# Kernel tuning notes

Hardware: AMD Instinct MI355X
Metric: run time of the kernel (lower is better)

The kernel has to match this reference:

```python
import jax, jax.numpy as jnp
import numpy as np

SEQ_LEN = 8
NUM_HEADS = 8
LN_EPS = 1e-5
GN_EPS = 64e-5  # GroupNorm eps = head_dim * 1e-5 (RWKV7 convention, head_dim=64)


def layer_norm(x, w, b):
    mu = x.mean(-1, keepdims=True)
    var = ((x - mu) ** 2).mean(-1, keepdims=True)
    return (x - mu) / jnp.sqrt(var + LN_EPS) * w + b


def token_shift(x):
    # delta = shift(x) - x; shift prepends one zero token along time
    return jnp.pad(x, ((0, 0), (1, 0), (0, 0)))[:, :-1] - x


def group_norm(x, w, b, H):
    B, T, C = x.shape
    xh = x.reshape(B, T, H, C // H)
    mu = xh.mean(-1, keepdims=True)
    var = ((xh - mu) ** 2).mean(-1, keepdims=True)
    return ((xh - mu) / jnp.sqrt(var + GN_EPS)).reshape(B, T, C) * w + b


def rwkv7_scan(r, w, k, v, a, b, H):
    # Generalized delta-rule recurrence (RWKV7):
    #   S_t = S_{t-1} * diag(exp(-exp(w_t))) + (S_{t-1} a_t) b_t^T + v_t k_t^T
    #   o_t = S_t r_t
    B, T, C = r.shape
    N = C // H

    def tm(x):  # [B,T,C] -> [T,B,H,N] (time-major for scan)
        return x.reshape(B, T, H, N).transpose(1, 0, 2, 3)

    decay = jnp.exp(-jnp.exp(tm(w)))
    rs, ks, vs, as_, bs = tm(r), tm(k), tm(v), tm(a), tm(b)

    def step(S, inp):
        rt, dt, kt, vt, at, bt = inp  # each [B,H,N]
        sa = jnp.einsum('bhij,bhj->bhi', S, at)
        S = (S * dt[:, :, None, :]
             + sa[..., None] * bt[:, :, None, :]
             + vt[..., None] * kt[:, :, None, :])
        return S, jnp.einsum('bhij,bhj->bhi', S, rt)

    S0 = jnp.zeros((B, H, N, N), r.dtype)
    _, out = jax.lax.scan(step, S0, (rs, decay, ks, vs, as_, bs))
    return out.transpose(1, 0, 2, 3).reshape(B, T, C)


def _forward(image_tensor, pos_emb, xm, w0, w1, w2, a0, a1, a2, v0, v1, v2,
             g1, g2, kkp, kap, rkp, Wr, Wk, Wv, Wo, lnx_w, lnx_b,
             ln1_w, ln1_b, ln2_w, ln2_b, fxk, Wkey, Wval, lnf_w, lnf_b):
    EB, C, ih, iw = image_tensor.shape
    B = EB // SEQ_LEN
    H = NUM_HEADS
    x = image_tensor.transpose(0, 2, 3, 1).reshape(EB, ih * iw, C)
    x = (x + pos_emb).reshape(B, SEQ_LEN * ih * iw, C)  # [B, T, C]
    L = Wr.shape[0]
    v_first = None
    for l in range(L):
        # ---- time mix (RWKV7 attention) ----
        h = layer_norm(x, ln1_w[l], ln1_b[l])
        Bh, T, _ = h.shape
        dx = token_shift(h)
        xr, xw, xk, xv, xa, xg = [h + dx * xm[l, i] for i in range(6)]
        r = xr @ Wr[l]
        w = -jax.nn.softplus(-(w0[l] + jnp.tanh(xw @ w1[l]) @ w2[l])) - 0.5
        k = xk @ Wk[l]
        v = xv @ Wv[l]
        if v_first is None:
            v_first = v
        else:
            v = v + (v_first - v) * jax.nn.sigmoid(v0[l] + (xv @ v1[l]) @ v2[l])
        a = jax.nn.sigmoid(a0[l] + (xa @ a1[l]) @ a2[l])  # in-context lr
        g = jax.nn.sigmoid(xg @ g1[l]) @ g2[l]
        kk = (k * kkp[l]).reshape(Bh, T, H, -1)
        kk = kk / jnp.maximum(jnp.linalg.norm(kk, axis=-1, keepdims=True), 1e-12)
        kk = kk.reshape(Bh, T, C)
        k = k * (1.0 + (a - 1.0) * kap[l])
        o = rwkv7_scan(r, w, k, v, -kk, kk * a, H)
        o = group_norm(o, lnx_w[l], lnx_b[l], H)
        r4, k4, v4 = (t.reshape(Bh, T, H, -1) for t in (r, k, v))
        o = o + ((r4 * k4 * rkp[l]).sum(-1, keepdims=True) * v4).reshape(Bh, T, C)
        x = x + (o * g) @ Wo[l]
        # ---- channel mix (squared-ReLU FFN) ----
        h = layer_norm(x, ln2_w[l], ln2_b[l])
        kf = h + token_shift(h) * fxk[l]
        x = x + jnp.square(jax.nn.relu(kf @ Wkey[l])) @ Wval[l]
    x = layer_norm(x, lnf_w, lnf_b)
    return x.reshape(EB, ih, iw, C).transpose(0, 3, 1, 2)


def setup_inputs() -> dict:
    key = jax.random.key(0)
    ks = jax.random.split(key, 24)
    L, C, H = 8, 512, 8
    DW, DA, DV, DG, FF = 64, 64, 32, 128, 2048
    EB, IV, IW = 32, 8, 16
    FS = IV * IW

    def n(k, shape, s=0.02):
        return jax.random.normal(k, shape, jnp.float32) * s

    return dict(
        image_tensor=jax.random.normal(ks[0], (EB, C, IV, IW), jnp.float32),
        pos_emb=n(ks[1], (1, FS, C)),
        xm=jax.random.uniform(ks[2], (L, 6, C), jnp.float32),
        w0=n(ks[3], (L, C), 0.5) - 0.5,
        w1=n(ks[4], (L, C, DW), 0.02), w2=n(ks[5], (L, DW, C), 0.1),
        a0=jnp.zeros((L, C), jnp.float32),
        a1=n(ks[6], (L, C, DA)), a2=n(ks[7], (L, DA, C), 0.1),
        v0=jnp.ones((L, C), jnp.float32),
        v1=n(ks[8], (L, C, DV)), v2=n(ks[9], (L, DV, C), 0.1),
        g1=n(ks[10], (L, C, DG)), g2=n(ks[11], (L, DG, C), 0.1),
        kkp=jnp.full((L, C), 0.85, jnp.float32),
        kap=jnp.ones((L, C), jnp.float32),
        rkp=n(ks[12], (L, H, C // H), 0.3),
        Wr=n(ks[13], (L, C, C)), Wk=n(ks[14], (L, C, C)),
        Wv=n(ks[15], (L, C, C)), Wo=n(ks[16], (L, C, C)),
        lnx_w=jnp.ones((L, C), jnp.float32), lnx_b=jnp.zeros((L, C), jnp.float32),
        ln1_w=jnp.ones((L, C), jnp.float32), ln1_b=jnp.zeros((L, C), jnp.float32),
        ln2_w=jnp.ones((L, C), jnp.float32), ln2_b=jnp.zeros((L, C), jnp.float32),
        fxk=jax.random.uniform(ks[17], (L, C), jnp.float32),
        Wkey=n(ks[18], (L, C, FF)), Wval=n(ks[19], (L, FF, C)),
        lnf_w=jnp.ones((C,), jnp.float32), lnf_b=jnp.zeros((C,), jnp.float32),
    )


def reference(image_tensor, pos_emb, xm, w0, w1, w2, a0, a1, a2, v0, v1, v2,
              g1, g2, kkp, kap, rkp, Wr, Wk, Wv, Wo, lnx_w, lnx_b,
              ln1_w, ln1_b, ln2_w, ln2_b, fxk, Wkey, Wval, lnf_w, lnf_b):
    return _forward(image_tensor, pos_emb, xm, w0, w1, w2, a0, a1, a2, v0, v1,
                    v2, g1, g2, kkp, kap, rkp, Wr, Wk, Wv, Wo, lnx_w, lnx_b,
                    ln1_w, ln1_b, ln2_w, ln2_b, fxk, Wkey, Wval, lnf_w, lnf_b)
```

## Files before the change

### kernel.cpp

```cpp
#include <hip/hip_runtime.h>
#include <hip/hip_bf16.h>
#include <math.h>


#define NTOK 4096
#define CDIM 512
#define TT   1024
#define LC   64
#define NCH  16
#define TB   8

#define BM 128
#define BK 32

enum { EPI_NONE=0, EPI_TANH, EPI_SIG, EPI_DECAY, EPI_SIGB, EPI_VMIX, EPI_RELU2, EPI_ADD };

typedef short bf16x8 __attribute__((ext_vector_type(8)));
typedef float f32x4 __attribute__((ext_vector_type(4)));
typedef unsigned short ushort_t;

__device__ __forceinline__ float wsum64(float v) {
#pragma unroll
  for (int s = 1; s < 64; s <<= 1) v += __shfl_xor(v, s);
  return v;
// ... 100 lines not shown
  if (nk > 1) STAGE(1, BK);
  int bc = 0, bs = 2;
  for (int k = 0; k + 1 < nk; ++k) {
    asm volatile("s_waitcnt vmcnt(%0)" :: "i"(LPW) : "memory");
    __builtin_amdgcn_s_barrier();
    if (k + 2 < nk) {
      STAGE(bs, (k + 2) * BK);
      bs = (bs == 2) ? 0 : bs + 1;
    }
    COMPUTE(bc);
    bc = (bc == 2) ? 0 : bc + 1;
  }
  asm volatile("s_waitcnt vmcnt(0)" ::: "memory");
  __builtin_amdgcn_s_barrier();
  COMPUTE(bc);
#undef STAGE
#undef COMPUTE

  void* Cout = sg.C;
  const float* bias = sg.bias;
  const float* e1 = sg.e1;
  const int em = m0 + wm + ((lane >> 4) << 2);
  const int en = n0 + wn + (lane & 15);

#define EPI_STORE(EPI_, OBF_)                                                 \
  { _Pragma("unroll") for (int fi = 0; fi < 4; ++fi) {                        \
      _Pragma("unroll") for (int fj = 0; fj < WNF; ++fj) {                    \
        const int gn = en + fj * 16;                                          \
        if (gn < N) {                                                         \
          _Pragma("unroll") for (int rr = 0; rr < 4; ++rr) {                  \
            const int gm = em + fi * 16 + rr;                                 \
            const size_t idx = (size_t)gm * N + gn;                           \
            const float y = acc[fi][fj][rr];                                  \
            float outv;                                                       \
            if (EPI_ == EPI_NONE) { outv = y; }                               \
            else if (EPI_ == EPI_TANH) { outv = tanhf(y); }                   \
            else if (EPI_ == EPI_SIG) { outv = sigm(y); }                     \
            else if (EPI_ == EPI_DECAY) {                                     \
              const float z = bias[gn] + y;                                   \
              const float w = -log1pf(expf(-z)) - 0.5f;                       \
              outv = expf(-expf(w));                                          \
            } else if (EPI_ == EPI_SIGB) { outv = sigm(bias[gn] + y); }       \
            else if (EPI_ == EPI_VMIX) {                                      \
              const float vr = ((float*)Cout)[idx];                           \
              outv = vr + (e1[idx] - vr) * sigm(bias[gn] + y);                \
            } else if (EPI_ == EPI_RELU2) {                                   \
              const float t = fmaxf(y, 0.f); outv = t * t;                    \
            } else { outv = ((float*)Cout)[idx] + y; }                        \
            if (OBF_) ((ushort_t*)Cout)[idx] = f2bf(outv);                    \
            else      ((float*)Cout)[idx] = outv;                             \
          }                                                                   \
        }                                                                     \
      } } }

  switch (sg.epi) {
    case EPI_NONE:  if (sg.obf) EPI_STORE(EPI_NONE, 1) else EPI_STORE(EPI_NONE, 0); break;
    case EPI_TANH:  EPI_STORE(EPI_TANH, 1); break;
    case EPI_SIG:   EPI_STORE(EPI_SIG, 1); break;
    case EPI_DECAY: EPI_STORE(EPI_DECAY, 0); break;
    case EPI_SIGB:  EPI_STORE(EPI_SIGB, 0); break;
    case EPI_VMIX:  EPI_STORE(EPI_VMIX, 0); break;
    case EPI_RELU2: EPI_STORE(EPI_RELU2, 1); break;
    case EPI_ADD:   EPI_STORE(EPI_ADD, 0); break;
  }
#undef EPI_STORE
}

__global__ __launch_bounds__(256) void wprep_k(
    const float* __restrict__ in, ushort_t* __restrict__ out,
    int K, int N, int Npad)
{
  __shared__ float t[32][33];
  const int l = blockIdx.z;
  const int n0 = blockIdx.x * 32, k0 = blockIdx.y * 32;
  const int tx = threadIdx.x & 31, ty = threadIdx.x >> 5;
  const float* src = in + (size_t)l * K * N;
  ushort_t* dst = out + (size_t)l * Npad * K;
#pragma unroll
  for (int i = 0; i < 32; i += 8) {
    const int k = k0 + ty + i, n = n0 + tx;
    t[ty + i][tx] = (n < N) ? src[(size_t)k * N + n] : 0.f;
  }
  __syncthreads();
#pragma unroll
  for (int i = 0; i < 32; i += 8) {
    const int n = n0 + ty + i, k = k0 + tx;
    dst[(size_t)n * K + k] = f2bf(t[tx][ty + i]);
  }
}

__global__ __launch_bounds__(256) void lnmix6_k(
    const float* __restrict__ x, const float* __restrict__ w,
    const float* __restrict__ b, const float* __restrict__ xml,
    ushort_t* __restrict__ xr, ushort_t* __restrict__ xw,
    ushort_t* __restrict__ xk, ushort_t* __restrict__ xv,
    ushort_t* __restrict__ xa, ushort_t* __restrict__ xg)
{
  const int m = blockIdx.x * 4 + (threadIdx.x >> 6);
  const int lane = threadIdx.x & 63;
  const int c0 = lane << 3;
  const size_t idx = (size_t)m * CDIM + c0;
  const bool first = ((m & (TT - 1)) == 0);
  float v[8], p[8];
  *(float4*)&v[0] = *(const float4*)&x[idx];
  *(float4*)&v[4] = *(const float4*)&x[idx + 4];
  if (first) {
#pragma unroll
    for (int j = 0; j < 8; ++j) p[j] = 0.f;
  } else {
    *(float4*)&p[0] = *(const float4*)&x[idx - CDIM];
    *(float4*)&p[4] = *(const float4*)&x[idx - CDIM + 4];
  }
  float s = 0.f, sp = 0.f;
#pragma unroll
  for (int j = 0; j < 8; ++j) { s += v[j]; sp += p[j]; }
  s = wsum64(s); sp = wsum64(sp);
  const float mu = s * (1.f / 512.f), mup = sp * (1.f / 512.f);
  float q = 0.f, qp = 0.f;
#pragma unroll
  for (int j = 0; j < 8; ++j) {
    const float d1 = v[j] - mu, d2 = p[j] - mup;
    q += d1 * d1; qp += d2 * d2;
  }
  q = wsum64(q); qp = wsum64(qp);
  const float is = rsqrtf(q * (1.f / 512.f) + 1e-5f);
  const float isp = rsqrtf(qp * (1.f / 512.f) + 1e-5f);
  float wc[8], bc[8];
  *(float4*)&wc[0] = *(const float4*)&w[c0]; *(float4*)&wc[4] = *(const float4*)&w[c0 + 4];
  *(float4*)&bc[0] = *(const float4*)&b[c0]; *(float4*)&bc[4] = *(const float4*)&b[c0 + 4];
  float hv[8], dx[8];
#pragma unroll
  for (int j = 0; j < 8; ++j) {
    hv[j] = (v[j] - mu) * is * wc[j] + bc[j];
    const float hp = first ? 0.f : (p[j] - mup) * isp * wc[j] + bc[j];
    dx[j] = hp - hv[j];
  }
  ushort_t* outs[6] = {xr, xw, xk, xv, xa, xg};
#pragma unroll
  for (int o = 0; o < 6; ++o) {
    float mc[8];
    *(float4*)&mc[0] = *(const float4*)&xml[o * CDIM + c0];
    *(float4*)&mc[4] = *(const float4*)&xml[o * CDIM + c0 + 4];
    bf16x8 pk;
#pragma unroll
    for (int j = 0; j < 8; ++j) pk[j] = (short)f2bf(fmaf(dx[j], mc[j], hv[j]));
    *(bf16x8*)&outs[o][idx] = pk;
  }
}

__global__ __launch_bounds__(256) void lnmix1_k(
    const float* __restrict__ x, const float* __restrict__ w,
    const float* __restrict__ b, const float* __restrict__ coef,
    ushort_t* __restrict__ kf)
{
  const int m = blockIdx.x * 4 + (threadIdx.x >> 6);
  const int lane = threadIdx.x & 63;
  const int c0 = lane << 3;
  const size_t idx = (size_t)m * CDIM + c0;
  const bool first = ((m & (TT - 1)) == 0);
  float v[8], p[8];
  *(float4*)&v[0] = *(const float4*)&x[idx];
  *(float4*)&v[4] = *(const float4*)&x[idx + 4];
  if (first) {
#pragma unroll
    for (int j = 0; j < 8; ++j) p[j] = 0.f;
  } else {
    *(float4*)&p[0] = *(const float4*)&x[idx - CDIM];
    *(float4*)&p[4] = *(const float4*)&x[idx - CDIM + 4];
  }
  float s = 0.f, sp = 0.f;
#pragma unroll
  for (int j = 0; j < 8; ++j) { s += v[j]; sp += p[j]; }
  s = wsum64(s); sp = wsum64(sp);
  const float mu = s * (1.f / 512.f), mup = sp * (1.f / 512.f);
  float q = 0.f, qp = 0.f;
#pragma unroll
  for (int j = 0; j < 8; ++j) {
    const float d1 = v[j] - mu, d2 = p[j] - mup;
    q += d1 * d1; qp += d2 * d2;
  }
  q = wsum64(q); qp = wsum64(qp);
  const float is = rsqrtf(q * (1.f / 512.f) + 1e-5f);
  const float isp = rsqrtf(qp * (1.f / 512.f) + 1e-5f);
  bf16x8 pk;
#pragma unroll
  for (int j = 0; j < 8; ++j) {
    const float wc = w[c0 + j], bc = b[c0 + j];
    const float hv = (v[j] - mu) * is * wc + bc;
    const float hp = first ? 0.f : (p[j] - mup) * isp * wc + bc;
    pk[j] = (short)f2bf(fmaf(hp - hv, coef[c0 + j], hv));
  }
  *(bf16x8*)&kf[idx] = pk;
}

__global__ __launch_bounds__(256) void prep_k(
    float* __restrict__ k, const float* __restrict__ a,
    const float* __restrict__ kkp, const float* __restrict__ kap,
    float* __restrict__ aa, float* __restrict__ bb)
{
  const int m = blockIdx.x * 4 + (threadIdx.x >> 6);
  const int lane = threadIdx.x & 63;
  const int c0 = lane << 3;
  const size_t idx = (size_t)m * CDIM + c0;
  float kv[8], av[8], kp[8], ka[8];
  *(float4*)&kv[0] = *(const float4*)&k[idx];     *(float4*)&kv[4] = *(const float4*)&k[idx + 4];
  *(float4*)&av[0] = *(const float4*)&a[idx];     *(float4*)&av[4] = *(const float4*)&a[idx + 4];
  *(float4*)&kp[0] = *(const float4*)&kkp[c0];    *(float4*)&kp[4] = *(const float4*)&kkp[c0 + 4];
  *(float4*)&ka[0] = *(const float4*)&kap[c0];    *(float4*)&ka[4] = *(const float4*)&kap[c0 + 4];
  float kk[8], ss = 0.f;
#pragma unroll
  for (int j = 0; j < 8; ++j) { kk[j] = kv[j] * kp[j]; ss += kk[j] * kk[j]; }
  ss = gsum8(ss);
  const float rden = 1.f / fmaxf(sqrtf(ss), 1e-12f);
  float oaa[8], obb[8], okk[8];
#pragma unroll
  for (int j = 0; j < 8; ++j) {
    const float kkn = kk[j] * rden;
    oaa[j] = -kkn;
    obb[j] = kkn * av[j];
    okk[j] = kv[j] * (1.f + (av[j] - 1.f) * ka[j]);
  }
  *(float4*)&aa[idx] = *(float4*)&oaa[0]; *(float4*)&aa[idx + 4] = *(float4*)&oaa[4];
  *(float4*)&bb[idx] = *(float4*)&obb[0]; *(float4*)&bb[idx + 4] = *(float4*)&obb[4];
  *(float4*)&k[idx]  = *(float4*)&okk[0]; *(float4*)&k[idx + 4]  = *(float4*)&okk[4];
}

__global__ __launch_bounds__(256) void post_k(
    const float* __restrict__ o, const float* __restrict__ r,
    const float* __restrict__ k, const float* __restrict__ v,
    const float* __restrict__ g, const float* __restrict__ gw,
    const float* __restrict__ gb, const float* __restrict__ rkp,
    ushort_t* __restrict__ og)
{
  const int m = blockIdx.x * 4 + (threadIdx.x >> 6);
  const int lane = threadIdx.x & 63;
  const int c0 = lane << 3;
  const size_t idx = (size_t)m * CDIM + c0;
  float ov[8], rv[8], kv[8], vv[8], gv[8], rp[8];
  *(float4*)&ov[0] = *(const float4*)&o[idx];   *(float4*)&ov[4] = *(const float4*)&o[idx + 4];
  *(float4*)&rv[0] = *(const float4*)&r[idx];   *(float4*)&rv[4] = *(const float4*)&r[idx + 4];
  *(float4*)&kv[0] = *(const float4*)&k[idx];   *(float4*)&kv[4] = *(const float4*)&k[idx + 4];
  *(float4*)&vv[0] = *(const float4*)&v[idx];   *(float4*)&vv[4] = *(const float4*)&v[idx + 4];
  *(float4*)&gv[0] = *(const float4*)&g[idx];   *(float4*)&gv[4] = *(const float4*)&g[idx + 4];
  *(float4*)&rp[0] = *(const float4*)&rkp[c0];  *(float4*)&rp[4] = *(const float4*)&rkp[c0 + 4];
  float s = 0.f, dot = 0.f;
#pragma unroll
  for (int j = 0; j < 8; ++j) { s += ov[j]; dot += rv[j] * kv[j] * rp[j]; }
  s = gsum8(s); dot = gsum8(dot);
  const float mu = s * (1.f / 64.f);
  float q = 0.f;
#pragma unroll
  for (int j = 0; j < 8; ++j) { const float d = ov[j] - mu; q += d * d; }
  q = gsum8(q);
  const float is = rsqrtf(q * (1.f / 64.f) + 64e-5f);
  bf16x8 pk;
#pragma unroll
  for (int j = 0; j < 8; ++j) {
    const float gn = (ov[j] - mu) * is * gw[c0 + j] + gb[c0 + j];
    pk[j] = (short)f2bf((gn + dot * vv[j]) * gv[j]);
  }
  *(bf16x8*)&og[idx] = pk;
}

__global__ __launch_bounds__(512) void ln_final_k(
    const float* __restrict__ x, const float* __restrict__ w,
    const float* __restrict__ b, float* __restrict__ out)
{
  const int m = blockIdx.x, c = threadIdx.x;
  const size_t idx = (size_t)m * CDIM + c;
  const float v = x[idx];
  __shared__ float red[8], red2[8];
  float s = wsum64(v);
  if ((c & 63) == 0) red[c >> 6] = s;
  __syncthreads();
  float tot = 0.f;
#pragma unroll
  for (int u = 0; u < 8; ++u) tot += red[u];
  const float mu = tot * (1.f / 512.f);
  const float dv = v - mu;
  float s2 = wsum64(dv * dv);
  if ((c & 63) == 0) red2[c >> 6] = s2;
  __syncthreads();
  float vt = 0.f;
#pragma unroll
  for (int u = 0; u < 8; ++u) vt += red2[u];
  const float y = dv * rsqrtf(vt * (1.f / 512.f) + 1e-5f) * w[c] + b[c];
  const int bidx = m >> 10, t = m & 1023;
  const int p = t & 127, eb = bidx * 8 + (t >> 7);
  out[((size_t)eb * CDIM + c) * 128 + p] = y;
}

__global__ __launch_bounds__(512) void build_x_k(
    const float* __restrict__ img, const float* __restrict__ pos,
    float* __restrict__ x)
{
  const int m = blockIdx.x, c = threadIdx.x;
  const int bidx = m >> 10, t = m & 1023;
  const int p = t & 127, eb = bidx * 8 + (t >> 7);
  x[(size_t)m * CDIM + c] =
      img[((size_t)eb * CDIM + c) * 128 + p] + pos[(size_t)p * CDIM + c];
}

__global__ __launch_bounds__(256) void scan1_k(
    const float* __restrict__ d, const float* __restrict__ k,
    const float* __restrict__ v, const float* __restrict__ aa,
    const float* __restrict__ bb,
    float* __restrict__ P, float* __restrict__ Q)
{
  const int ch = blockIdx.x, bh = blockIdx.y;
  const int b = bh >> 3, hh = bh & 7;
  const int tid = threadIdx.x;
  const int rg = tid >> 4, cg = tid & 15;
  const int r0 = rg << 2, c0 = cg << 2;
  float S[16], Pr[16];
#pragma unroll
  for (int ri = 0; ri < 4; ++ri)
#pragma unroll
    for (int cj = 0; cj < 4; ++cj) {
      S[ri * 4 + cj] = 0.f;
      Pr[ri * 4 + cj] = (r0 + ri == c0 + cj) ? 1.f : 0.f;
    }

  __shared__ float sbuf[3][5 * TB * 64];
  const size_t base = (size_t)b * TT * CDIM + (size_t)ch * LC * CDIM + hh * 64;
  const float* srcs[5] = {d, k, v, aa, bb};
  const int f0 = tid, f1 = tid + 256, f2 = tid + 512;
  const float* gp0 = srcs[f0 >> 7] + base + (size_t)((f0 >> 4) & 7) * CDIM + ((f0 & 15) << 2);
  const float* gp1 = srcs[f1 >> 7] + base + (size_t)((f1 >> 4) & 7) * CDIM + ((f1 & 15) << 2);
  const float* gp2 = (tid < 128)
      ? srcs[f2 >> 7] + base + (size_t)((f2 >> 4) & 7) * CDIM + ((f2 & 15) << 2)
      : srcs[0];

#define STAGE1(bf_, goff_)                                     \
  {                                                            \
    glds16(gp0 + (goff_), &sbuf[bf_][f0 << 2]);                \
    glds16(gp1 + (goff_), &sbuf[bf_][f1 << 2]);                \
    if (tid < 128) glds16(gp2 + (goff_), &sbuf[bf_][f2 << 2]); \
  }

#define CGRP1(bf_)                                                              \
  {                                                                             \
    const float* sb0 = sbuf[bf_];                                               \
    _Pragma("unroll") for (int tt = 0; tt < TB; ++tt) {                         \
      const float* sd  = sb0 + 0 * TB * 64 + tt * 64;                           \
      const float* sk  = sb0 + 1 * TB * 64 + tt * 64;                           \
      const float* sv  = sb0 + 2 * TB * 64 + tt * 64;                           \
      const float* sa  = sb0 + 3 * TB * 64 + tt * 64;                           \
      const float* sbv = sb0 + 4 * TB * 64 + tt * 64;                           \
      const float4 a4 = *(const float4*)(sa + c0);                              \
      const float4 d4 = *(const float4*)(sd + c0);                              \
      const float4 k4 = *(const float4*)(sk + c0);                              \
      const float4 b4 = *(const float4*)(sbv + c0);                             \
      const float4 v4 = *(const float4*)(sv + r0);                              \
      const float dd[4] = {d4.x, d4.y, d4.z, d4.w};                             \
      const float ak[4] = {a4.x, a4.y, a4.z, a4.w};                             \
      const float kc[4] = {k4.x, k4.y, k4.z, k4.w};                             \
      const float bc2[4] = {b4.x, b4.y, b4.z, b4.w};                            \
      const float vr[4] = {v4.x, v4.y, v4.z, v4.w};                             \
      float ps[4], pp[4];                                                       \
      _Pragma("unroll") for (int ri = 0; ri < 4; ++ri) {                        \
        ps[ri] = fmaf(S[ri*4+0], ak[0], fmaf(S[ri*4+1], ak[1],                  \
                 fmaf(S[ri*4+2], ak[2], S[ri*4+3] * ak[3])));                   \
        pp[ri] = fmaf(Pr[ri*4+0], ak[0], fmaf(Pr[ri*4+1], ak[1],                \
                 fmaf(Pr[ri*4+2], ak[2], Pr[ri*4+3] * ak[3])));                 \
      }                                                                         \
      _Pragma("unroll") for (int ri = 0; ri < 4; ++ri) {                        \
        ps[ri] = rowsum16(ps[ri]);                                              \
        pp[ri] = rowsum16(pp[ri]);                                              \
      }                                                                         \
      _Pragma("unroll") for (int ri = 0; ri < 4; ++ri)                          \
        _Pragma("unroll") for (int cj = 0; cj < 4; ++cj) {                      \
          S[ri*4+cj]  = fmaf(S[ri*4+cj], dd[cj],                                \
                        fmaf(ps[ri], bc2[cj], vr[ri] * kc[cj]));                \
          Pr[ri*4+cj] = fmaf(Pr[ri*4+cj], dd[cj], pp[ri] * bc2[cj]);            \
        }                                                                       \
    }                                                                           \
  }

  constexpr int NG = LC / TB;
  STAGE1(0, 0);
  STAGE1(1, (size_t)TB * CDIM);
  int bc = 0, bs = 2;
  for (int g = 0; g + 1 < NG; ++g) {
    if (tid < 128) { asm volatile("s_waitcnt vmcnt(3)" ::: "memory"); }
    else           { asm volatile("s_waitcnt vmcnt(2)" ::: "memory"); }
    __builtin_amdgcn_s_barrier();
    if (g + 2 < NG) {
      STAGE1(bs, (size_t)(g + 2) * TB * CDIM);
      bs = (bs == 2) ? 0 : bs + 1;
    }
    CGRP1(bc);
    bc = (bc == 2) ? 0 : bc + 1;
  }
  asm volatile("s_waitcnt vmcnt(0)" ::: "memory");
  __builtin_amdgcn_s_barrier();
  CGRP1(bc);
#undef STAGE1
#undef CGRP1

  const size_t ob = ((size_t)(bh * NCH + ch)) * 4096 + (size_t)r0 * 64 + c0;
#pragma unroll
  for (int ri = 0; ri < 4; ++ri) {
    *(float4*)&Q[ob + ri * 64] = make_float4(S[ri*4+0], S[ri*4+1], S[ri*4+2], S[ri*4+3]);
    *(float4*)&P[ob + ri * 64] = make_float4(Pr[ri*4+0], Pr[ri*4+1], Pr[ri*4+2], Pr[ri*4+3]);
  }
}

__global__ __launch_bounds__(512) void scan2_k(
    const float* __restrict__ P, const float* __restrict__ Q,
    float* __restrict__ Sst)
{
  const int tid = threadIdx.x;
  const int f0 = tid << 2;
  const int r0 = tid >> 4;
  const int c0 = (tid & 15) << 2;
  __shared__ float sP[4096];
  __shared__ float sS[4096];
  float4 S0 = {0.f, 0.f, 0.f, 0.f}, S1 = {0.f, 0.f, 0.f, 0.f};
  const size_t cbase = (size_t)blockIdx.x * NCH * 4096;
  float4 pf0 = *(const float4*)&P[cbase + f0];
  float4 pf1 = *(const float4*)&P[cbase + f0 + 2048];

  for (int c = 0; c < NCH; ++c) {
    const size_t cb = cbase + (size_t)c * 4096;
    *(float4*)&Sst[cb + f0] = S0;
    *(float4*)&Sst[cb + f0 + 2048] = S1;
    __syncthreads();
    *(float4*)&sP[f0] = pf0;  *(float4*)&sP[f0 + 2048] = pf1;
    *(float4*)&sS[f0] = S0;   *(float4*)&sS[f0 + 2048] = S1;
    __syncthreads();
    if (c + 1 < NCH) {
      pf0 = *(const float4*)&P[cb + 4096 + f0];
      pf1 = *(const float4*)&P[cb + 4096 + f0 + 2048];
    }
    const float4 q0 = *(const float4*)&Q[cb + f0];
    const float4 q1 = *(const float4*)&Q[cb + f0 + 2048];

    float a00 = 0.f, a01 = 0.f, a02 = 0.f, a03 = 0.f;
    float a10 = 0.f, a11 = 0.f, a12 = 0.f, a13 = 0.f;
    const float* sS0 = &sS[r0 * 64];
    const float* sS1 = &sS[(r0 + 32) * 64];
#pragma unroll
    for (int mm = 0; mm < 64; ++mm) {
      const float4 p4 = *(const float4*)&sP[mm * 64 + c0];
      const float u0 = sS0[mm], u1 = sS1[mm];
      a00 = fmaf(u0, p4.x, a00); a01 = fmaf(u0, p4.y, a01);
      a02 = fmaf(u0, p4.z, a02); a03 = fmaf(u0, p4.w, a03);
      a10 = fmaf(u1, p4.x, a10); a11 = fmaf(u1, p4.y, a11);
      a12 = fmaf(u1, p4.z, a12); a13 = fmaf(u1, p4.w, a13);
    }
    S0.x = a00 + q0.x; S0.y = a01 + q0.y; S0.z = a02 + q0.z; S0.w = a03 + q0.w;
    S1.x = a10 + q1.x; S1.y = a11 + q1.y; S1.z = a12 + q1.z; S1.w = a13 + q1.w;
  }
}

__global__ __launch_bounds__(256) void scan3_k(
    const float* __restrict__ r, const float* __restrict__ d,
    const float* __restrict__ k, const float* __restrict__ v,
    const float* __restrict__ aa, const float* __restrict__ bb,
    const float* __restrict__ Sst, float* __restrict__ o)
{
  const int ch = blockIdx.x, bh = blockIdx.y;
  const int b = bh >> 3, hh = bh & 7;
  const int tid = threadIdx.x;
  const int rg = tid >> 4, cg = tid & 15;
  const int r0 = rg << 2, c0 = cg << 2;
  float S[16];
  const size_t sb_ = ((size_t)(bh * NCH + ch)) * 4096 + (size_t)r0 * 64 + c0;
#pragma unroll
  for (int ri = 0; ri < 4; ++ri) {
    const float4 s4 = *(const float4*)&Sst[sb_ + ri * 64];
    S[ri*4+0] = s4.x; S[ri*4+1] = s4.y; S[ri*4+2] = s4.z; S[ri*4+3] = s4.w;
  }

  __shared__ float sbuf[3][6 * TB * 64];
  const size_t base = (size_t)b * TT * CDIM + (size_t)ch * LC * CDIM + hh * 64;
  const float* srcs[6] = {r, d, k, v, aa, bb};
  const int f0 = tid, f1 = tid + 256, f2 = tid + 512;
  const float* gp0 = srcs[f0 >> 7] + base + (size_t)((f0 >> 4) & 7) * CDIM + ((f0 & 15) << 2);
  const float* gp1 = srcs[f1 >> 7] + base + (size_t)((f1 >> 4) & 7) * CDIM + ((f1 & 15) << 2);
  const float* gp2 = srcs[f2 >> 7] + base + (size_t)((f2 >> 4) & 7) * CDIM + ((f2 & 15) << 2);

#define STAGE3(bf_, goff_)                          \
  {                                                 \
    glds16(gp0 + (goff_), &sbuf[bf_][f0 << 2]);     \
    glds16(gp1 + (goff_), &sbuf[bf_][f1 << 2]);     \
    glds16(gp2 + (goff_), &sbuf[bf_][f2 << 2]);     \
  }

#define CGRP3(bf_, g_)                                                          \
  {                                                                             \
    const float* sb0 = sbuf[bf_];                                               \
    const size_t obase = base + (size_t)(g_) * TB * CDIM;                       \
    _Pragma("unroll") for (int tt = 0; tt < TB; ++tt) {                         \
      const float* sr  = sb0 + 0 * TB * 64 + tt * 64;                           \
      const float* sd  = sb0 + 1 * TB * 64 + tt * 64;                           \
      const float* sk  = sb0 + 2 * TB * 64 + tt * 64;                           \
      const float* sv  = sb0 + 3 * TB * 64 + tt * 64;                           \
      const float* sa  = sb0 + 4 * TB * 64 + tt * 64;                           \
      const float* sbv = sb0 + 5 * TB * 64 + tt * 64;                           \
      const float4 a4 = *(const float4*)(sa + c0);                              \
      const float4 d4 = *(const float4*)(sd + c0);                              \
      const float4 k4 = *(const float4*)(sk + c0);                              \
      const float4 b4 = *(const float4*)(sbv + c0);                             \
      const float4 r4 = *(const float4*)(sr + c0);                              \
      const float4 v4 = *(const float4*)(sv + r0);                              \
      const float dd[4] = {d4.x, d4.y, d4.z, d4.w};                             \
      const float ak[4] = {a4.x, a4.y, a4.z, a4.w};                             \
      const float kc[4] = {k4.x, k4.y, k4.z, k4.w};                             \
      const float bc2[4] = {b4.x, b4.y, b4.z, b4.w};                            \
      const float rr[4] = {r4.x, r4.y, r4.z, r4.w};                             \
      const float vr[4] = {v4.x, v4.y, v4.z, v4.w};                             \
      float ps[4];                                                              \
      _Pragma("unroll") for (int ri = 0; ri < 4; ++ri)                          \
        ps[ri] = fmaf(S[ri*4+0], ak[0], fmaf(S[ri*4+1], ak[1],                  \
                 fmaf(S[ri*4+2], ak[2], S[ri*4+3] * ak[3])));                   \
      _Pragma("unroll") for (int ri = 0; ri < 4; ++ri)                          \
        ps[ri] = rowsum16(ps[ri]);                                              \
      float po[4];                                                              \
      _Pragma("unroll") for (int ri = 0; ri < 4; ++ri) {                        \
        float acc_ = 0.f;                                                       \
        _Pragma("unroll") for (int cj = 0; cj < 4; ++cj) {                      \
          const float sn = fmaf(S[ri*4+cj], dd[cj],                             \
                           fmaf(ps[ri], bc2[cj], vr[ri] * kc[cj]));             \
          S[ri*4+cj] = sn;                                                      \
          acc_ = fmaf(sn, rr[cj], acc_);                                        \
        }                                                                       \
        po[ri] = acc_;                                                          \
      }                                                                         \
      _Pragma("unroll") for (int ri = 0; ri < 4; ++ri)                          \
        po[ri] = rowsum16(po[ri]);                                              \
      if (cg == 0) {                                                            \
        float4 po4 = make_float4(po[0], po[1], po[2], po[3]);                   \
        *(float4*)&o[obase + (size_t)tt * CDIM + r0] = po4;                     \
      }                                                                         \
    }                                                                           \
  }

  constexpr int NG = LC / TB;
  STAGE3(0, 0);
  STAGE3(1, (size_t)TB * CDIM);
  int bc = 0, bs = 2;
  for (int g = 0; g + 1 < NG; ++g) {
    asm volatile("s_waitcnt vmcnt(3)" ::: "memory");
    __builtin_amdgcn_s_barrier();
    if (g + 2 < NG) {
      STAGE3(bs, (size_t)(g + 2) * TB * CDIM);
      bs = (bs == 2) ? 0 : bs + 1;
    }
    CGRP3(bc, g);
    bc = (bc == 2) ? 0 : bc + 1;
  }
  asm volatile("s_waitcnt vmcnt(0)" ::: "memory");
  __builtin_amdgcn_s_barrier();
  CGRP3(bc, NG - 1);
#undef STAGE3
#undef CGRP3
}

extern "C" void kernel_launch(void* const* d_in, const int* in_sizes, int n_in,
                              void* d_out, int out_size, void* d_ws, size_t ws_size,
                              hipStream_t stream) {
  (void)in_sizes; (void)n_in; (void)out_size; (void)ws_size;
  const float* img  = (const float*)d_in[0];
  const float* pos  = (const float*)d_in[1];
  const float* xm   = (const float*)d_in[2];
  const float* w0   = (const float*)d_in[3];
  const float* w1   = (const float*)d_in[4];
  const float* w2   = (const float*)d_in[5];
  const float* a0   = (const float*)d_in[6];
  const float* a1   = (const float*)d_in[7];
  const float* a2   = (const float*)d_in[8];
  const float* v0   = (const float*)d_in[9];
  const float* v1   = (const float*)d_in[10];
  const float* v2   = (const float*)d_in[11];
  const float* g1   = (const float*)d_in[12];
  const float* g2   = (const float*)d_in[13];
  const float* kkp  = (const float*)d_in[14];
  const float* kap  = (const float*)d_in[15];
  const float* rkp  = (const float*)d_in[16];
  const float* Wr   = (const float*)d_in[17];
  const float* Wk   = (const float*)d_in[18];
  const float* Wv   = (const float*)d_in[19];
  const float* Wo   = (const float*)d_in[20];
  const float* lnxw = (const float*)d_in[21];
  const float* lnxb = (const float*)d_in[22];
  const float* ln1w = (const float*)d_in[23];
  const float* ln1b = (const float*)d_in[24];
  const float* ln2w = (const float*)d_in[25];
  const float* ln2b = (const float*)d_in[26];
  const float* fxk  = (const float*)d_in[27];
  const float* Wkey = (const float*)d_in[28];
  const float* Wval = (const float*)d_in[29];
  const float* lnfw = (const float*)d_in[30];
  const float* lnfb = (const float*)d_in[31];

  float* ws = (float*)d_ws;
  const size_t SZ = (size_t)NTOK * CDIM;
  float* x   = ws + 0 * SZ;
  float* r_  = ws + 2 * SZ;
  float* dec = ws + 3 * SZ;
  float* k_  = ws + 4 * SZ;
  float* v_  = ws + 5 * SZ;
  float* vf  = ws + 6 * SZ;
  float* a_  = ws + 7 * SZ;
  float* g_  = ws + 8 * SZ;
  float* aa  = ws + 9 * SZ;
  float* bb  = ws + 10 * SZ;
  float* o_  = ws + 11 * SZ;
  float* mixf = ws + 12 * SZ;
  ushort_t* xr = (ushort_t*)mixf;
  ushort_t* xw = xr + SZ;
  ushort_t* xk = xr + 2 * SZ;
  ushort_t* xv = xr + 3 * SZ;
  ushort_t* xa = xr + 4 * SZ;
  ushort_t* xg = xr + 5 * SZ;
  float* Pbuf = mixf;
  float* Qbuf = mixf + SZ;
  float* Sst  = mixf + 2 * SZ;
  ushort_t* tmpb = (ushort_t*)(ws + 15 * SZ);
  ushort_t* t0b = tmpb;
  ushort_t* t1b = tmpb + (size_t)NTOK * 64;
  ushort_t* t2b = tmpb + (size_t)NTOK * 128;
  ushort_t* t3b = tmpb + (size_t)NTOK * 160;
  ushort_t* tfb  = (ushort_t*)(ws + 15 * SZ + SZ / 2);
  ushort_t* ogb  = (ushort_t*)(ws + 17 * SZ + SZ / 2);
  ushort_t* wb   = (ushort_t*)(ws + 18 * SZ);

  const size_t oWr  = 0;
  const size_t oWk  = oWr  + (size_t)8 * 512 * 512;
  const size_t oWv  = oWk  + (size_t)8 * 512 * 512;
  const size_t oWo  = oWv  + (size_t)8 * 512 * 512;
  const size_t oW1  = oWo  + (size_t)8 * 512 * 512;
  const size_t oW2  = oW1  + (size_t)8 * 128 * 512;
  const size_t oA1  = oW2  + (size_t)8 * 512 * 64;
  const size_t oA2  = oA1  + (size_t)8 * 128 * 512;
  const size_t oV1  = oA2  + (size_t)8 * 512 * 64;
  const size_t oV2  = oV1  + (size_t)8 * 128 * 512;
  const size_t oG1  = oV2  + (size_t)8 * 512 * 32;
  const size_t oG2  = oG1  + (size_t)8 * 128 * 512;
  const size_t oKey = oG2  + (size_t)8 * 512 * 128;
  const size_t oVal = oKey + (size_t)8 * 2048 * 512;

#define WPREP(src, dst, K_, N_, NP_) \
  wprep_k<<<dim3((NP_) / 32, (K_) / 32, 8), 256, 0, stream>>>(src, dst, K_, N_, NP_)
  WPREP(Wr,   wb + oWr,  512, 512, 512);
  WPREP(Wk,   wb + oWk,  512, 512, 512);
  WPREP(Wv,   wb + oWv,  512, 512, 512);
  WPREP(Wo,   wb + oWo,  512, 512, 512);
  WPREP(w1,   wb + oW1,  512, 64,  128);
  WPREP(w2,   wb + oW2,  64,  512, 512);
  WPREP(a1,   wb + oA1,  512, 64,  128);
  WPREP(a2,   wb + oA2,  64,  512, 512);
  WPREP(v1,   wb + oV1,  512, 32,  128);
  WPREP(v2,   wb + oV2,  32,  512, 512);
  WPREP(g1,   wb + oG1,  512, 128, 128);
  WPREP(g2,   wb + oG2,  128, 512, 512);
  WPREP(Wkey, wb + oKey, 512, 2048, 2048);
  WPREP(Wval, wb + oVal, 2048, 512, 512);
#undef WPREP

  build_x_k<<<NTOK, 512, 0, stream>>>(img, pos, x);

  for (int l = 0; l < 8; ++l) {
    const size_t lc = (size_t)l * CDIM;
    const float* xml = xm + (size_t)l * 6 * CDIM;
    const ushort_t* bWr = wb + oWr + (size_t)l * 512 * 512;
    const ushort_t* bWk = wb + oWk + (size_t)l * 512 * 512;
    const ushort_t* bWv = wb + oWv + (size_t)l * 512 * 512;
    const ushort_t* bWo = wb + oWo + (size_t)l * 512 * 512;
    const ushort_t* bW1 = wb + oW1 + (size_t)l * 128 * 512;
    const ushort_t* bW2 = wb + oW2 + (size_t)l * 512 * 64;
    const ushort_t* bA1 = wb + oA1 + (size_t)l * 128 * 512;
    const ushort_t* bA2 = wb + oA2 + (size_t)l * 512 * 64;
    const ushort_t* bV1 = wb + oV1 + (size_t)l * 128 * 512;
    const ushort_t* bV2 = wb + oV2 + (size_t)l * 512 * 32;
    const ushort_t* bG1 = wb + oG1 + (size_t)l * 128 * 512;
    const ushort_t* bG2 = wb + oG2 + (size_t)l * 512 * 128;
    const ushort_t* bKy = wb + oKey + (size_t)l * 2048 * 512;
    const ushort_t* bVl = wb + oVal + (size_t)l * 512 * 2048;
    float* vdst = (l == 0) ? vf : v_;

    lnmix6_k<<<NTOK / 4, 256, 0, stream>>>(x, ln1w + lc, ln1b + lc, xml,
                                           xr, xw, xk, xv, xa, xg);
    Segs4 qkv;
    qkv.s[0] = {xr, bWr, r_,   0, 0, 512, 512, EPI_NONE, 0};
    qkv.s[1] = {xk, bWk, k_,   0, 0, 512, 512, EPI_NONE, 0};
    qkv.s[2] = {xv, bWv, vdst, 0, 0, 512, 512, EPI_NONE, 0};
    qkv.s[3] = {0, 0, 0, 0, 0, 0, 0, -1, 0};
    ggemm_k<64><<<dim3(NTOK / BM, 8, 3), 256, 0, stream>>>(qkv);

    Segs4 dn;
    dn.s[0] = {xw, bW1, t0b, 0, 0, 64,  512, EPI_TANH, 1};
    dn.s[1] = {xa, bA1, t1b, 0, 0, 64,  512, EPI_NONE, 1};
    dn.s[2] = {xv, bV1, t2b, 0, 0, 32,  512, EPI_NONE, 1};
    dn.s[3] = {xg, bG1, t3b, 0, 0, 128, 512, EPI_SIG,  1};
    ggemm_k<64><<<dim3(NTOK / BM, 2, 4), 256, 0, stream>>>(dn);

    Segs4 up;
    up.s[0] = {t0b, bW2, dec, w0 + lc, 0,  512, 64,  EPI_DECAY, 0};
    up.s[1] = {t1b, bA2, a_,  a0 + lc, 0,  512, 64,  EPI_SIGB,  0};
    up.s[2] = {t2b, bV2, v_,  v0 + lc, vf, 512, 32,  (l > 0) ? EPI_VMIX : -1, 0};
    up.s[3] = {t3b, bG2, g_,  0, 0,        512, 128, EPI_NONE,  0};
    ggemm_k<64><<<dim3(NTOK / BM, 8, 4), 256, 0, stream>>>(up);

    const float* vptr = (l == 0) ? vf : v_;
    prep_k<<<NTOK / 4, 256, 0, stream>>>(k_, a_, kkp + lc, kap + lc, aa, bb);
    scan1_k<<<dim3(NCH, 32), 256, 0, stream>>>(dec, k_, vptr, aa, bb, Pbuf, Qbuf);
    scan2_k<<<32, 512, 0, stream>>>(Pbuf, Qbuf, Sst);
    scan3_k<<<dim3(NCH, 32), 256, 0, stream>>>(r_, dec, k_, vptr, aa, bb, Sst, o_);
    post_k<<<NTOK / 4, 256, 0, stream>>>(o_, r_, k_, vptr, g_, lnxw + lc, lnxb + lc,
                                         rkp + lc, ogb);
    Segs4 wo;
    wo.s[0] = {ogb, bWo, x, 0, 0, 512, 512, EPI_ADD, 0};
    wo.s[1] = wo.s[2] = wo.s[3] = {0, 0, 0, 0, 0, 0, 0, -1, 0};
    ggemm_k<64><<<dim3(NTOK / BM, 8, 1), 256, 0, stream>>>(wo);

    lnmix1_k<<<NTOK / 4, 256, 0, stream>>>(x, ln2w + lc, ln2b + lc, fxk + lc, xr);
    Segs4 f1;
    f1.s[0] = {xr, bKy, tfb, 0, 0, 2048, 512, EPI_RELU2, 1};
    f1.s[1] = f1.s[2] = f1.s[3] = {0, 0, 0, 0, 0, 0, 0, -1, 0};
    ggemm_k<64><<<dim3(NTOK / BM, 32, 1), 256, 0, stream>>>(f1);
    Segs4 f2;
    f2.s[0] = {tfb, bVl, x, 0, 0, 512, 2048, EPI_ADD, 0};
    f2.s[1] = f2.s[2] = f2.s[3] = {0, 0, 0, 0, 0, 0, 0, -1, 0};
    ggemm_k<64><<<dim3(NTOK / BM, 8, 1), 256, 0, stream>>>(f2);
  }

  ln_final_k<<<NTOK, 512, 0, stream>>>(x, lnfw, lnfb, (float*)d_out);
}
```

Measured before the change: 2.182 ms.

## Fuse local-output computation into chunk scan and replace rescan with correction matmul

The first chunked-scan pass now also computes the zero-initial-state outputs o and a projected transition Y = P^T r per timestep, so the third pass no longer re-runs the full recurrence. A new correction kernel adds Y·S_start to o with a small 64x64 matmul per chunk. This removes one full sequential recurrence pass and its input reload, at the cost of extra rowsum work in pass one, an extra Y buffer and an extra read-modify-write of o.

```diff
diff --git a/kernel.cpp b/kernel.cpp
--- a/kernel.cpp
+++ b/kernel.cpp
@@ -426,10 +426,11 @@
 }
 
 __global__ __launch_bounds__(256) void scan1_k(
-    const float* __restrict__ d, const float* __restrict__ k,
-    const float* __restrict__ v, const float* __restrict__ aa,
-    const float* __restrict__ bb,
-    float* __restrict__ P, float* __restrict__ Q)
+    const float* __restrict__ r, const float* __restrict__ d,
+    const float* __restrict__ k, const float* __restrict__ v,
+    const float* __restrict__ aa, const float* __restrict__ bb,
+    float* __restrict__ P, float* __restrict__ Q,
+    float* __restrict__ Y, float* __restrict__ o)
 {
   const int ch = blockIdx.x, bh = blockIdx.y;
   const int b = bh >> 3, hh = bh & 7;
@@ -444,158 +445,6 @@
       S[ri * 4 + cj] = 0.f;
       Pr[ri * 4 + cj] = (r0 + ri == c0 + cj) ? 1.f : 0.f;
     }
-
-  __shared__ float sbuf[3][5 * TB * 64];
-  const size_t base = (size_t)b * TT * CDIM + (size_t)ch * LC * CDIM + hh * 64;
-  const float* srcs[5] = {d, k, v, aa, bb};
-  const int f0 = tid, f1 = tid + 256, f2 = tid + 512;
-  const float* gp0 = srcs[f0 >> 7] + base + (size_t)((f0 >> 4) & 7) * CDIM + ((f0 & 15) << 2);
-  const float* gp1 = srcs[f1 >> 7] + base + (size_t)((f1 >> 4) & 7) * CDIM + ((f1 & 15) << 2);
-  const float* gp2 = (tid < 128)
-      ? srcs[f2 >> 7] + base + (size_t)((f2 >> 4) & 7) * CDIM + ((f2 & 15) << 2)
-      : srcs[0];
-
-#define STAGE1(bf_, goff_)                                     \
-  {                                                            \
-    glds16(gp0 + (goff_), &sbuf[bf_][f0 << 2]);                \
-    glds16(gp1 + (goff_), &sbuf[bf_][f1 << 2]);                \
-    if (tid < 128) glds16(gp2 + (goff_), &sbuf[bf_][f2 << 2]); \
-  }
-
-#define CGRP1(bf_)                                                              \
-  {                                                                             \
-    const float* sb0 = sbuf[bf_];                                               \
-    _Pragma("unroll") for (int tt = 0; tt < TB; ++tt) {                         \
-      const float* sd  = sb0 + 0 * TB * 64 + tt * 64;                           \
-      const float* sk  = sb0 + 1 * TB * 64 + tt * 64;                           \
-      const float* sv  = sb0 + 2 * TB * 64 + tt * 64;                           \
-      const float* sa  = sb0 + 3 * TB * 64 + tt * 64;                           \
-      const float* sbv = sb0 + 4 * TB * 64 + tt * 64;                           \
-      const float4 a4 = *(const float4*)(sa + c0);                              \
-      const float4 d4 = *(const float4*)(sd + c0);                              \
-      const float4 k4 = *(const float4*)(sk + c0);                              \
-      const float4 b4 = *(const float4*)(sbv + c0);                             \
-      const float4 v4 = *(const float4*)(sv + r0);                              \
-      const float dd[4] = {d4.x, d4.y, d4.z, d4.w};                             \
-      const float ak[4] = {a4.x, a4.y, a4.z, a4.w};                             \
-      const float kc[4] = {k4.x, k4.y, k4.z, k4.w};                             \
-      const float bc2[4] = {b4.x, b4.y, b4.z, b4.w};                            \
-      const float vr[4] = {v4.x, v4.y, v4.z, v4.w};                             \
-      float ps[4], pp[4];                                                       \
-      _Pragma("unroll") for (int ri = 0; ri < 4; ++ri) {                        \
-        ps[ri] = fmaf(S[ri*4+0], ak[0], fmaf(S[ri*4+1], ak[1],                  \
-                 fmaf(S[ri*4+2], ak[2], S[ri*4+3] * ak[3])));                   \
-        pp[ri] = fmaf(Pr[ri*4+0], ak[0], fmaf(Pr[ri*4+1], ak[1],                \
-                 fmaf(Pr[ri*4+2], ak[2], Pr[ri*4+3] * ak[3])));                 \
-      }                                                                         \
-      _Pragma("unroll") for (int ri = 0; ri < 4; ++ri) {                        \
-        ps[ri] = rowsum16(ps[ri]);                                              \
-        pp[ri] = rowsum16(pp[ri]);                                              \
-      }                                                                         \
-      _Pragma("unroll") for (int ri = 0; ri < 4; ++ri)                          \
-        _Pragma("unroll") for (int cj = 0; cj < 4; ++cj) {                      \
-          S[ri*4+cj]  = fmaf(S[ri*4+cj], dd[cj],                                \
-                        fmaf(ps[ri], bc2[cj], vr[ri] * kc[cj]));                \
-          Pr[ri*4+cj] = fmaf(Pr[ri*4+cj], dd[cj], pp[ri] * bc2[cj]);            \
-        }                                                                       \
-    }                                                                           \
-  }
-
-  constexpr int NG = LC / TB;
-  STAGE1(0, 0);
-  STAGE1(1, (size_t)TB * CDIM);
-  int bc = 0, bs = 2;
-  for (int g = 0; g + 1 < NG; ++g) {
-    if (tid < 128) { asm volatile("s_waitcnt vmcnt(3)" ::: "memory"); }
-    else           { asm volatile("s_waitcnt vmcnt(2)" ::: "memory"); }
-    __builtin_amdgcn_s_barrier();
-    if (g + 2 < NG) {
-      STAGE1(bs, (size_t)(g + 2) * TB * CDIM);
-      bs = (bs == 2) ? 0 : bs + 1;
-    }
-    CGRP1(bc);
-    bc = (bc == 2) ? 0 : bc + 1;
-  }
-  asm volatile("s_waitcnt vmcnt(0)" ::: "memory");
-  __builtin_amdgcn_s_barrier();
-  CGRP1(bc);
-#undef STAGE1
-#undef CGRP1
-
-  const size_t ob = ((size_t)(bh * NCH + ch)) * 4096 + (size_t)r0 * 64 + c0;
-#pragma unroll
-  for (int ri = 0; ri < 4; ++ri) {
-    *(float4*)&Q[ob + ri * 64] = make_float4(S[ri*4+0], S[ri*4+1], S[ri*4+2], S[ri*4+3]);
-    *(float4*)&P[ob + ri * 64] = make_float4(Pr[ri*4+0], Pr[ri*4+1], Pr[ri*4+2], Pr[ri*4+3]);
-  }
-}
-
-__global__ __launch_bounds__(512) void scan2_k(
-    const float* __restrict__ P, const float* __restrict__ Q,
-    float* __restrict__ Sst)
-{
-  const int tid = threadIdx.x;
-  const int f0 = tid << 2;
-  const int r0 = tid >> 4;
-  const int c0 = (tid & 15) << 2;
-  __shared__ float sP[4096];
-  __shared__ float sS[4096];
-  float4 S0 = {0.f, 0.f, 0.f, 0.f}, S1 = {0.f, 0.f, 0.f, 0.f};
-  const size_t cbase = (size_t)blockIdx.x * NCH * 4096;
-  float4 pf0 = *(const float4*)&P[cbase + f0];
-  float4 pf1 = *(const float4*)&P[cbase + f0 + 2048];
-
-  for (int c = 0; c < NCH; ++c) {
-    const size_t cb = cbase + (size_t)c * 4096;
-    *(float4*)&Sst[cb + f0] = S0;
-    *(float4*)&Sst[cb + f0 + 2048] = S1;
-    __syncthreads();
-    *(float4*)&sP[f0] = pf0;  *(float4*)&sP[f0 + 2048] = pf1;
-    *(float4*)&sS[f0] = S0;   *(float4*)&sS[f0 + 2048] = S1;
-    __syncthreads();
-    if (c + 1 < NCH) {
-      pf0 = *(const float4*)&P[cb + 4096 + f0];
-      pf1 = *(const float4*)&P[cb + 4096 + f0 + 2048];
-    }
-    const float4 q0 = *(const float4*)&Q[cb + f0];
-    const float4 q1 = *(const float4*)&Q[cb + f0 + 2048];
-
-    float a00 = 0.f, a01 = 0.f, a02 = 0.f, a03 = 0.f;
-    float a10 = 0.f, a11 = 0.f, a12 = 0.f, a13 = 0.f;
-    const float* sS0 = &sS[r0 * 64];
-    const float* sS1 = &sS[(r0 + 32) * 64];
-#pragma unroll
-    for (int mm = 0; mm < 64; ++mm) {
-      const float4 p4 = *(const float4*)&sP[mm * 64 + c0];
-      const float u0 = sS0[mm], u1 = sS1[mm];
-      a00 = fmaf(u0, p4.x, a00); a01 = fmaf(u0, p4.y, a01);
-      a02 = fmaf(u0, p4.z, a02); a03 = fmaf(u0, p4.w, a03);
-      a10 = fmaf(u1, p4.x, a10); a11 = fmaf(u1, p4.y, a11);
-      a12 = fmaf(u1, p4.z, a12); a13 = fmaf(u1, p4.w, a13);
-    }
-    S0.x = a00 + q0.x; S0.y = a01 + q0.y; S0.z = a02 + q0.z; S0.w = a03 + q0.w;
-    S1.x = a10 + q1.x; S1.y = a11 + q1.y; S1.z = a12 + q1.z; S1.w = a13 + q1.w;
-  }
-}
-
-__global__ __launch_bounds__(256) void scan3_k(
-    const float* __restrict__ r, const float* __restrict__ d,
-    const float* __restrict__ k, const float* __restrict__ v,
-    const float* __restrict__ aa, const float* __restrict__ bb,
-    const float* __restrict__ Sst, float* __restrict__ o)
-{
-  const int ch = blockIdx.x, bh = blockIdx.y;
-  const int b = bh >> 3, hh = bh & 7;
-  const int tid = threadIdx.x;
-  const int rg = tid >> 4, cg = tid & 15;
-  const int r0 = rg << 2, c0 = cg << 2;
-  float S[16];
-  const size_t sb_ = ((size_t)(bh * NCH + ch)) * 4096 + (size_t)r0 * 64 + c0;
-#pragma unroll
-  for (int ri = 0; ri < 4; ++ri) {
-    const float4 s4 = *(const float4*)&Sst[sb_ + ri * 64];
-    S[ri*4+0] = s4.x; S[ri*4+1] = s4.y; S[ri*4+2] = s4.z; S[ri*4+3] = s4.w;
-  }
 
   __shared__ float sbuf[3][6 * TB * 64];
   const size_t base = (size_t)b * TT * CDIM + (size_t)ch * LC * CDIM + hh * 64;
@@ -604,18 +453,20 @@
   const float* gp0 = srcs[f0 >> 7] + base + (size_t)((f0 >> 4) & 7) * CDIM + ((f0 & 15) << 2);
   const float* gp1 = srcs[f1 >> 7] + base + (size_t)((f1 >> 4) & 7) * CDIM + ((f1 & 15) << 2);
   const float* gp2 = srcs[f2 >> 7] + base + (size_t)((f2 >> 4) & 7) * CDIM + ((f2 & 15) << 2);
-
-#define STAGE3(bf_, goff_)                          \
+  const size_t ybase0 = ((size_t)(bh * NCH + ch)) * 4096;
+
+#define STAGE1(bf_, goff_)                          \
   {                                                 \
     glds16(gp0 + (goff_), &sbuf[bf_][f0 << 2]);     \
     glds16(gp1 + (goff_), &sbuf[bf_][f1 << 2]);     \
     glds16(gp2 + (goff_), &sbuf[bf_][f2 << 2]);     \
   }
 
-#define CGRP3(bf_, g_)                                                          \
+#define CGRP1(bf_, g_)                                                          \
   {                                                                             \
     const float* sb0 = sbuf[bf_];                                               \
     const size_t obase = base + (size_t)(g_) * TB * CDIM;                       \
+    const size_t ybase = ybase0 + (size_t)(g_) * TB * 64;                       \
     _Pragma("unroll") for (int tt = 0; tt < TB; ++tt) {                         \
       const float* sr  = sb0 + 0 * TB * 64 + tt * 64;                           \
       const float* sd  = sb0 + 1 * TB * 64 + tt * 64;                           \
@@ -635,51 +486,164 @@
       const float bc2[4] = {b4.x, b4.y, b4.z, b4.w};                            \
       const float rr[4] = {r4.x, r4.y, r4.z, r4.w};                             \
       const float vr[4] = {v4.x, v4.y, v4.z, v4.w};                             \
-      float ps[4];                                                              \
-      _Pragma("unroll") for (int ri = 0; ri < 4; ++ri)                          \
+      float ps[4], pp[4];                                                       \
+      _Pragma("unroll") for (int ri = 0; ri < 4; ++ri) {                        \
         ps[ri] = fmaf(S[ri*4+0], ak[0], fmaf(S[ri*4+1], ak[1],                  \
                  fmaf(S[ri*4+2], ak[2], S[ri*4+3] * ak[3])));                   \
-      _Pragma("unroll") for (int ri = 0; ri < 4; ++ri)                          \
+        pp[ri] = fmaf(Pr[ri*4+0], ak[0], fmaf(Pr[ri*4+1], ak[1],                \
+                 fmaf(Pr[ri*4+2], ak[2], Pr[ri*4+3] * ak[3])));                 \
+      }                                                                         \
+      _Pragma("unroll") for (int ri = 0; ri < 4; ++ri) {                        \
         ps[ri] = rowsum16(ps[ri]);                                              \
-      float po[4];                                                              \
+        pp[ri] = rowsum16(pp[ri]);                                              \
+      }                                                                         \
+      float yv[4], ol[4];                                                       \
       _Pragma("unroll") for (int ri = 0; ri < 4; ++ri) {                        \
-        float acc_ = 0.f;                                                       \
+        float yacc = 0.f, oacc = 0.f;                                           \
         _Pragma("unroll") for (int cj = 0; cj < 4; ++cj) {                      \
           const float sn = fmaf(S[ri*4+cj], dd[cj],                             \
                            fmaf(ps[ri], bc2[cj], vr[ri] * kc[cj]));             \
+          const float pn = fmaf(Pr[ri*4+cj], dd[cj], pp[ri] * bc2[cj]);         \
           S[ri*4+cj] = sn;                                                      \
-          acc_ = fmaf(sn, rr[cj], acc_);                                        \
+          Pr[ri*4+cj] = pn;                                                     \
+          oacc = fmaf(sn, rr[cj], oacc);                                        \
+          yacc = fmaf(pn, rr[cj], yacc);                                        \
         }                                                                       \
-        po[ri] = acc_;                                                          \
+        ol[ri] = oacc; yv[ri] = yacc;                                           \
       }                                                                         \
-      _Pragma("unroll") for (int ri = 0; ri < 4; ++ri)                          \
-        po[ri] = rowsum16(po[ri]);                                              \
+      _Pragma("unroll") for (int ri = 0; ri < 4; ++ri) {                        \
+        ol[ri] = rowsum16(ol[ri]);                                              \
+        yv[ri] = rowsum16(yv[ri]);                                              \
+      }                                                                         \
       if (cg == 0) {                                                            \
-        float4 po4 = make_float4(po[0], po[1], po[2], po[3]);                   \
-        *(float4*)&o[obase + (size_t)tt * CDIM + r0] = po4;                     \
+        *(float4*)&o[obase + (size_t)tt * CDIM + r0] =                          \
+            make_float4(ol[0], ol[1], ol[2], ol[3]);                            \
+        *(float4*)&Y[ybase + (size_t)tt * 64 + r0] =                            \
+            make_float4(yv[0], yv[1], yv[2], yv[3]);                            \
       }                                                                         \
     }                                                                           \
   }
 
   constexpr int NG = LC / TB;
-  STAGE3(0, 0);
-  STAGE3(1, (size_t)TB * CDIM);
+  STAGE1(0, 0);
+  STAGE1(1, (size_t)TB * CDIM);
   int bc = 0, bs = 2;
   for (int g = 0; g + 1 < NG; ++g) {
     asm volatile("s_waitcnt vmcnt(3)" ::: "memory");
     __builtin_amdgcn_s_barrier();
     if (g + 2 < NG) {
-      STAGE3(bs, (size_t)(g + 2) * TB * CDIM);
+      STAGE1(bs, (size_t)(g + 2) * TB * CDIM);
       bs = (bs == 2) ? 0 : bs + 1;
     }
-    CGRP3(bc, g);
+    CGRP1(bc, g);
     bc = (bc == 2) ? 0 : bc + 1;
   }
   asm volatile("s_waitcnt vmcnt(0)" ::: "memory");
   __builtin_amdgcn_s_barrier();
-  CGRP3(bc, NG - 1);
-#undef STAGE3
-#undef CGRP3
+  CGRP1(bc, NG - 1);
+#undef STAGE1
+#undef CGRP1
+
+  const size_t ob = ybase0 + (size_t)r0 * 64 + c0;
+#pragma unroll
+  for (int ri = 0; ri < 4; ++ri) {
+    *(float4*)&Q[ob + ri * 64] = make_float4(S[ri*4+0], S[ri*4+1], S[ri*4+2], S[ri*4+3]);
+    *(float4*)&P[ob + ri * 64] = make_float4(Pr[ri*4+0], Pr[ri*4+1], Pr[ri*4+2], Pr[ri*4+3]);
+  }
+}
+
+__global__ __launch_bounds__(512) void scan2_k(
+    const float* __restrict__ P, const float* __restrict__ Q,
+    float* __restrict__ Sst)
+{
+  const int tid = threadIdx.x;
+  const int f0 = tid << 2;
+  const int r0 = tid >> 4;
+  const int c0 = (tid & 15) << 2;
+  __shared__ float sP[4096];
+  __shared__ float sS[4096];
+  float4 S0 = {0.f, 0.f, 0.f, 0.f}, S1 = {0.f, 0.f, 0.f, 0.f};
+  const size_t cbase = (size_t)blockIdx.x * NCH * 4096;
+  float4 pf0 = *(const float4*)&P[cbase + f0];
+  float4 pf1 = *(const float4*)&P[cbase + f0 + 2048];
+
+  for (int c = 0; c < NCH; ++c) {
+    const size_t cb = cbase + (size_t)c * 4096;
+    *(float4*)&Sst[cb + f0] = S0;
+    *(float4*)&Sst[cb + f0 + 2048] = S1;
+    __syncthreads();
+    *(float4*)&sP[f0] = pf0;  *(float4*)&sP[f0 + 2048] = pf1;
+    *(float4*)&sS[f0] = S0;   *(float4*)&sS[f0 + 2048] = S1;
+    __syncthreads();
+    if (c + 1 < NCH) {
+      pf0 = *(const float4*)&P[cb + 4096 + f0];
+      pf1 = *(const float4*)&P[cb + 4096 + f0 + 2048];
+    }
+    const float4 q0 = *(const float4*)&Q[cb + f0];
+    const float4 q1 = *(const float4*)&Q[cb + f0 + 2048];
+
+    float a00 = 0.f, a01 = 0.f, a02 = 0.f, a03 = 0.f;
+    float a10 = 0.f, a11 = 0.f, a12 = 0.f, a13 = 0.f;
+    const float* sS0 = &sS[r0 * 64];
+    const float* sS1 = &sS[(r0 + 32) * 64];
+#pragma unroll
+    for (int mm = 0; mm < 64; ++mm) {
+      const float4 p4 = *(const float4*)&sP[mm * 64 + c0];
+      const float u0 = sS0[mm], u1 = sS1[mm];
+      a00 = fmaf(u0, p4.x, a00); a01 = fmaf(u0, p4.y, a01);
+      a02 = fmaf(u0, p4.z, a02); a03 = fmaf(u0, p4.w, a03);
+      a10 = fmaf(u1, p4.x, a10); a11 = fmaf(u1, p4.y, a11);
+      a12 = fmaf(u1, p4.z, a12); a13 = fmaf(u1, p4.w, a13);
+    }
+    S0.x = a00 + q0.x; S0.y = a01 + q0.y; S0.z = a02 + q0.z; S0.w = a03 + q0.w;
+    S1.x = a10 + q1.x; S1.y = a11 + q1.y; S1.z = a12 + q1.z; S1.w = a13 + q1.w;
+  }
+}
+
+__global__ __launch_bounds__(256) void corr_k(
+    const float* __restrict__ Sst, const float* __restrict__ Y,
+    float* __restrict__ o)
+{
+  const int ch = blockIdx.x, bh = blockIdx.y;
+  const int b = bh >> 3, hh = bh & 7;
+  const int tid = threadIdx.x;
+  __shared__ float ST[64][68];
+  __shared__ float Yl[64][68];
+  const size_t cb = ((size_t)(bh * NCH + ch)) * 4096;
+#pragma unroll
+  for (int u = 0; u < 16; ++u) {
+    const int idx = tid + 256 * u;
+    ST[idx & 63][idx >> 6] = Sst[cb + idx];
+  }
+#pragma unroll
+  for (int u = 0; u < 4; ++u) {
+    const int fi = tid + 256 * u;
+    *(float4*)&Yl[fi >> 4][(fi & 15) << 2] = *(const float4*)&Y[cb + (size_t)fi * 4];
+  }
+  __syncthreads();
+  const int t = tid >> 2, q = tid & 3, i0 = q << 4;
+  f32x4 acc[4];
+#pragma unroll
+  for (int u = 0; u < 4; ++u) acc[u] = (f32x4){0.f, 0.f, 0.f, 0.f};
+  const float* yrow = &Yl[t][0];
+#pragma unroll 4
+  for (int j = 0; j < 64; ++j) {
+    const float yv = yrow[j];
+#pragma unroll
+    for (int u = 0; u < 4; ++u) {
+      const f32x4 s4 = *(const f32x4*)&ST[j][i0 + 4 * u];
+      acc[u] = {fmaf(yv, s4[0], acc[u][0]), fmaf(yv, s4[1], acc[u][1]),
+                fmaf(yv, s4[2], acc[u][2]), fmaf(yv, s4[3], acc[u][3])};
+    }
+  }
+  const size_t obase = (size_t)b * TT * CDIM + (size_t)ch * LC * CDIM + hh * 64 +
+                       (size_t)t * CDIM + i0;
+#pragma unroll
+  for (int u = 0; u < 4; ++u) {
+    float4 cur = *(const float4*)&o[obase + 4 * u];
+    cur.x += acc[u][0]; cur.y += acc[u][1]; cur.z += acc[u][2]; cur.w += acc[u][3];
+    *(float4*)&o[obase + 4 * u] = cur;
+  }
 }
 
 extern "C" void kernel_launch(void* const* d_in, const int* in_sizes, int n_in,
@@ -748,6 +712,7 @@
   ushort_t* t2b = tmpb + (size_t)NTOK * 128;
   ushort_t* t3b = tmpb + (size_t)NTOK * 160;
   ushort_t* tfb  = (ushort_t*)(ws + 15 * SZ + SZ / 2);
+  float* Ybuf = ws + 16 * SZ;
   ushort_t* ogb  = (ushort_t*)(ws + 17 * SZ + SZ / 2);
   ushort_t* wb   = (ushort_t*)(ws + 18 * SZ);
 
@@ -830,9 +795,10 @@
 
     const float* vptr = (l == 0) ? vf : v_;
     prep_k<<<NTOK / 4, 256, 0, stream>>>(k_, a_, kkp + lc, kap + lc, aa, bb);
-    scan1_k<<<dim3(NCH, 32), 256, 0, stream>>>(dec, k_, vptr, aa, bb, Pbuf, Qbuf);
+    scan1_k<<<dim3(NCH, 32), 256, 0, stream>>>(r_, dec, k_, vptr, aa, bb,
+                                               Pbuf, Qbuf, Ybuf, o_);
     scan2_k<<<32, 512, 0, stream>>>(Pbuf, Qbuf, Sst);
-    scan3_k<<<dim3(NCH, 32), 256, 0, stream>>>(r_, dec, k_, vptr, aa, bb, Sst, o_);
+    corr_k<<<dim3(NCH, 32), 256, 0, stream>>>(Sst, Ybuf, o_);
     post_k<<<NTOK / 4, 256, 0, stream>>>(o_, r_, k_, vptr, g_, lnxw + lc, lnxb + lc,
                                          rkp + lc, ogb);
     Segs4 wo;
```

Measured after the change: 2.187 ms. Within noise of the previous version (+0.2%).
